# Performance work log

Measured on AMD Instinct MI355X. Metric: run time of the kernel, lower is better.

## Reference

```python
import jax, jax.numpy as jnp
import numpy as np

N = 50000       # nodes
E = 1600000     # edges (before self-loops)
H = 4           # heads
C = 32          # channels per head
G = 64          # graphs in batch
NEG_SLOPE = 0.2


def gat_conv(x, src, dst, W, att_src, att_dst, bias):
    # x: [N, Fin]; W: [Fin, H*C]; att_*: [H, C]; bias: [H*C]
    h = (x @ W).reshape(N, H, C)                       # [N, H, C]
    a_src = jnp.einsum('nhc,hc->nh', h, att_src)       # [N, H]
    a_dst = jnp.einsum('nhc,hc->nh', h, att_dst)       # [N, H]
    e = a_src[src] + a_dst[dst]                        # [E', H]
    e = jax.nn.leaky_relu(e, NEG_SLOPE)
    # softmax over incoming edges of each destination node
    m = jax.ops.segment_max(e, dst, num_segments=N)    # [N, H]
    ex = jnp.exp(e - m[dst])
    denom = jax.ops.segment_sum(ex, dst, num_segments=N)  # [N, H]
    alpha = ex / (denom[dst] + 1e-16)                  # [E', H]
    msg = h[src] * alpha[:, :, None]                   # [E', H, C]
    out = jax.ops.segment_sum(msg, dst, num_segments=N)  # [N, H, C]
    return out.reshape(N, H * C) + bias


def setup_inputs() -> dict:
    key = jax.random.key(0)
    ks = jax.random.split(key, 12)
    x = jax.random.normal(ks[0], (N, 128), dtype=jnp.float32)
    edge_index = jax.random.randint(ks[1], (2, E), 0, N, dtype=jnp.int64)
    batch = jnp.sort(jax.random.randint(ks[2], (N,), 0, G, dtype=jnp.int64))
    s = 0.05
    return {
        'x': x,
        'edge_index': edge_index,
        'batch': batch,
        'W1': jax.random.normal(ks[3], (128, H * C), dtype=jnp.float32) * s,
        'att_src1': jax.random.normal(ks[4], (H, C), dtype=jnp.float32) * s,
        'att_dst1': jax.random.normal(ks[5], (H, C), dtype=jnp.float32) * s,
        'b1': jnp.zeros((H * C,), dtype=jnp.float32),
        'W2': jax.random.normal(ks[6], (H * C, H * C), dtype=jnp.float32) * s,
        'att_src2': jax.random.normal(ks[7], (H, C), dtype=jnp.float32) * s,
        'att_dst2': jax.random.normal(ks[8], (H, C), dtype=jnp.float32) * s,
        'b2': jnp.zeros((H * C,), dtype=jnp.float32),
        'fc_W': jax.random.normal(ks[9], (H * C, 8), dtype=jnp.float32) * s,
        'fc_b': jnp.zeros((8,), dtype=jnp.float32),
    }


def reference(x, edge_index, batch, W1, att_src1, att_dst1, b1,
              W2, att_src2, att_dst2, b2, fc_W, fc_b):
    # add self loops (PyG GATConv default)
    ar = jnp.arange(N, dtype=edge_index.dtype)
    src = jnp.concatenate([edge_index[0], ar])
    dst = jnp.concatenate([edge_index[1], ar])
    h = gat_conv(x, src, dst, W1, att_src1, att_dst1, b1)
    h = jax.nn.elu(h)
    h = gat_conv(h, src, dst, W2, att_src2, att_dst2, b2)
    # global mean pool over graphs
    sums = jax.ops.segment_sum(h, batch, num_segments=G)          # [G, HC]
    cnt = jax.ops.segment_sum(jnp.ones((N,), h.dtype), batch, num_segments=G)
    pooled = sums / jnp.maximum(cnt, 1.0)[:, None]
    logits = pooled @ fc_W + fc_b                                  # [G, 8]
    return jax.nn.log_softmax(logits, axis=1)
```

## Files before the change

### kernel.cpp

```cpp
#include <hip/hip_runtime.h>
#include <math.h>

#define HC 128
#define GG 64
#define NEG 0.2f
#define TILE 8192
#define BW 128
#define SLOT 8192
#define NBMAX 512
#define LDA 136

typedef __attribute__((ext_vector_type(8))) short short8;
typedef __attribute__((ext_vector_type(4))) float floatx4;
typedef __attribute__((ext_vector_type(2))) float floatx2;

static __device__ __forceinline__ float leaky(float x) { return x > 0.f ? x : NEG * x; }

static __device__ __forceinline__ unsigned short f2bf(float f) {
    unsigned u = __float_as_uint(f);
    u += 0x7FFF + ((u >> 16) & 1);
    return (unsigned short)(u >> 16);
}
static __device__ __forceinline__ float bf2f(unsigned short s) {
    return __uint_as_float(((unsigned)s) << 16);
}

#if __has_builtin(__builtin_amdgcn_cvt_pk_f32_fp8) && __has_builtin(__builtin_amdgcn_cvt_pk_fp8_f32)
template <bool HI>
static __device__ __forceinline__ floatx2 fp8pair(unsigned int w) {
    return __builtin_amdgcn_cvt_pk_f32_fp8((int)w, HI);
}
static __device__ __forceinline__ unsigned int f32x2_fp8(float a, float b) {
    return ((unsigned int)__builtin_amdgcn_cvt_pk_fp8_f32(a, b, 0, false)) & 0xFFFFu;
}
#else
static __device__ __forceinline__ float fp8one(unsigned v) {
    unsigned e = (v >> 3) & 15u, m = v & 7u;
    float mag = e ? __uint_as_float(((e + 120u) << 23) | (m << 20))
                  : (float)m * 0.001953125f;
    return (v & 0x80u) ? -mag : mag;
}
template <bool HI>
static __device__ __forceinline__ floatx2 fp8pair(unsigned int w) {
    unsigned h = HI ? (w >> 16) : w;
    floatx2 r; r.x = fp8one(h & 0xFFu); r.y = fp8one((h >> 8) & 0xFFu);
    return r;
}
static __device__ __forceinline__ unsigned fp8enc(float f) {
    unsigned u = __float_as_uint(f);
    unsigned s = (u >> 24) & 0x80u;
    float a = fabsf(f);
    if (a >= 448.f) return s | 0x7Eu;
    if (a < 0.015625f) {
        unsigned m = (unsigned)(int)rintf(a * 512.f);
        return s | m;
    }
    u = __float_as_uint(a);
    u += 0xFFFFFu + ((u >> 20) & 1u);
    unsigned e8 = (u >> 23) - 120u;
    if (e8 >= 16u) return s | 0x7Eu;
    return s | (e8 << 3) | ((u >> 20) & 7u);
}
static __device__ __forceinline__ unsigned int f32x2_fp8(float a, float b) {
    return fp8enc(a) | (fp8enc(b) << 8);
}
#endif

static __device__ __forceinline__ void acc16(floatx2* acc, float w, const uint4& d) {
    floatx2 w2 = {w, w};
    acc[0] += w2 * fp8pair<false>(d.x);
    acc[1] += w2 * fp8pair<true>(d.x);
    acc[2] += w2 * fp8pair<false>(d.y);
    acc[3] += w2 * fp8pair<true>(d.y);
    acc[4] += w2 * fp8pair<false>(d.z);
    acc[5] += w2 * fp8pair<true>(d.z);
    acc[6] += w2 * fp8pair<false>(d.w);
    acc[7] += w2 * fp8pair<true>(d.w);
}

__global__ __launch_bounds__(256) void setup_k(const float* __restrict__ W1,
                                               const float* __restrict__ W2,
                                               unsigned short* __restrict__ Wt1,
                                               unsigned short* __restrict__ Wt2,
                                               int* __restrict__ gbcur,
                                               const int* __restrict__ batch,
                                               int* __restrict__ node_end,
                                               int* __restrict__ row_start,
                                               int NB, int Nn, int M) {
    int i = blockIdx.x * 256 + threadIdx.x;
    if (i < NB) gbcur[i] = i * SLOT;
    if (i == 0) row_start[Nn] = M;
    if (i < 32768) {
        const float* W = (i >> 14) ? W2 : W1;
        unsigned short* Wt = (i >> 14) ? Wt2 : Wt1;
        int d = i & 16383;
        int j = d & 7;
        int m = (d >> 3) & 15;
        int qf = d >> 7;
        int q = qf & 3;
        int f = qf >> 2;
        int kb = f & 3;
        int ct = f >> 2;
        int n = ct * 16 + m;
        int k = kb * 32 + q * 8 + j;
        Wt[d] = f2bf(W[k * 128 + n]);
    }
    if (i < Nn) {
        int b = batch[i];
        if (i == 0) {
            for (int g = 0; g < b; g++) node_end[g] = 0;
        }
        int bn = (i + 1 < Nn) ? batch[i + 1] : GG;
        for (int g = b; g < bn; g++) node_end[g] = i + 1;
    }
}

__global__ __launch_bounds__(256) void fused_k(const int* __restrict__ ei,
                                               int* __restrict__ gbcur,
                                               unsigned int* __restrict__ staging,
                                               int E, int M, int NB, int NBIN,
                                               const float* __restrict__ X,
                                               const unsigned short* __restrict__ Wt,
                                               const float* __restrict__ att_s,
                                               const float* __restrict__ att_d,
                                               unsigned char* __restrict__ H8,
                                               float* __restrict__ a_src,
                                               float* __restrict__ a_dst,
                                               int n_rows) {
    __shared__ __align__(16) char smem[39040];
    const int tid = threadIdx.x;

    if ((int)blockIdx.x < NBIN) {
        unsigned int* reorder = (unsigned int*)smem;
        int* s_cnt  = (int*)(smem + 32768);
        int* s_off  = (int*)(smem + 34816);
        int* s_run  = (int*)(smem + 36864);
        int* s_wsum = (int*)(smem + 38912);
        int* s_carry= (int*)(smem + 38944);
        const int lane = tid & 63, wid = tid >> 6;
        const int tbase = blockIdx.x * TILE;
        const int tcnt = min(TILE, M - tbase);

        for (int i = tid; i < NB; i += 256) s_cnt[i] = 0;
        if (tid == 0) *s_carry = 0;
        __syncthreads();

        for (int t = tid; t < tcnt; t += 256) {
            int i = tbase + t;
            int dst = (i < E) ? ei[E + i] : (i - E);
            atomicAdd(&s_cnt[dst >> 7], 1);
        }
        __syncthreads();

        for (int base = 0; base < NB; base += 256) {
            int i = base + tid;
            int v = (i < NB) ? s_cnt[i] : 0;
            int incl = v;
            #pragma unroll
            for (int off = 1; off < 64; off <<= 1) {
                int u = __shfl_up(incl, off);
                if (lane >= off) incl += u;
            }
            if (lane == 63) s_wsum[wid] = incl;
            __syncthreads();
            if (tid == 0) {
                int a = 0;
                for (int w = 0; w < 4; w++) { int tv = s_wsum[w]; s_wsum[w] = a; a += tv; }
                s_wsum[4] = a;
            }
            __syncthreads();
            int excl = *s_carry + s_wsum[wid] + incl - v;
            if (i < NB) s_off[i] = excl;
            __syncthreads();
            if (tid == 0) *s_carry += s_wsum[4];
            __syncthreads();
        }

        for (int b = tid; b < NB; b += 256)
            s_run[b] = atomicAdd(&gbcur[b], s_cnt[b]);
        for (int b = tid; b < NB; b += 256) s_cnt[b] = s_off[b];
        __syncthreads();

        for (int t = tid; t < tcnt; t += 256) {
            int i = tbase + t;
            int src, dst;
            if (i < E) { src = ei[i]; dst = ei[E + i]; }
            else       { src = dst = i - E; }
            unsigned int p = ((unsigned int)dst << 16) | (unsigned int)src;
            int r = atomicAdd(&s_cnt[dst >> 7], 1);
            reorder[r] = p;
        }
        __syncthreads();

        for (int t = tid; t < tcnt; t += 256) {
            unsigned int p = reorder[t];
            int b = p >> 23;
            staging[s_run[b] + (t - s_off[b])] = p;
        }
    } else {
        unsigned short* As = (unsigned short*)smem;
        const int gb = blockIdx.x - NBIN;
        const int row0 = gb * 64;

        for (int i = tid; i < 2048; i += 256) {
            int r = i >> 5;
            int c4 = (i & 31) << 2;
            int gr = row0 + r;
            float4 v = (gr < n_rows) ? ((const float4*)&X[(size_t)gr * 128])[i & 31]
                                     : make_float4(0.f, 0.f, 0.f, 0.f);
            ushort4 bv = {f2bf(v.x), f2bf(v.y), f2bf(v.z), f2bf(v.w)};
            *(ushort4*)&As[r * LDA + c4] = bv;
        }
        __syncthreads();

        const int lane = tid & 63;
        const int wave = tid >> 6;
        const int m = lane & 15;
        const int quad = lane >> 4;
        const int wr = wave * 16;

        floatx4 acc[8];
        #pragma unroll
        for (int ct = 0; ct < 8; ct++) acc[ct] = (floatx4){0.f, 0.f, 0.f, 0.f};

        #pragma unroll
        for (int kb = 0; kb < 4; kb++) {
            short8 x0 = *(const short8*)&As[(wr + m) * LDA + kb * 32 + quad * 8];
            #pragma unroll
            for (int ct = 0; ct < 8; ct++) {
                short8 wf = *(const short8*)&Wt[(((ct * 4 + kb) * 4) + quad) * 128 + m * 8];
                acc[ct] = __builtin_amdgcn_mfma_f32_16x16x32_bf16(wf, x0, acc[ct], 0, 0, 0);
            }
        }

        const int q4 = quad * 4;
        int node = row0 + wr + m;
        bool vld = node < n_rows;
        float ps[4] = {0.f, 0.f, 0.f, 0.f};
        float pd[4] = {0.f, 0.f, 0.f, 0.f};
        #pragma unroll
        for (int ct = 0; ct < 8; ct++) {
            floatx4 v = acc[ct];
            int c0 = ct * 16 + q4;
            float4 avs = *(const float4*)&att_s[c0];
            float4 avd = *(const float4*)&att_d[c0];
            int h = ct >> 1;
            ps[h] += v[0] * avs.x + v[1] * avs.y + v[2] * avs.z + v[3] * avs.w;
            pd[h] += v[0] * avd.x + v[1] * avd.y + v[2] * avd.z + v[3] * avd.w;
            if (vld) {
                unsigned pk01 = f32x2_fp8(v[0], v[1]);
                unsigned pk23 = f32x2_fp8(v[2], v[3]);
                *(unsigned*)&H8[(size_t)node * 128 + c0] = pk01 | (pk23 << 16);
            }
        }
        #pragma unroll
        for (int h = 0; h < 4; h++) {
            ps[h] += __shfl_xor(ps[h], 16); ps[h] += __shfl_xor(ps[h], 32);
            pd[h] += __shfl_xor(pd[h], 16); pd[h] += __shfl_xor(pd[h], 32);
        }
        if (lane < 16 && vld) {
            float4 s4 = {ps[0], ps[1], ps[2], ps[3]};
            float4 d4 = {pd[0], pd[1], pd[2], pd[3]};
            *(float4*)&a_src[node * 4] = s4;
            *(float4*)&a_dst[node * 4] = d4;
        }
    }
}

__global__ __launch_bounds__(256) void unbin_k(const unsigned int* __restrict__ staging,
                                               const int* __restrict__ gbcur,
                                               int* __restrict__ row_start,
                                               unsigned short* __restrict__ srcs, int Nn) {
    __shared__ int s_cnt[BW];
    __shared__ int s_cur[BW];
    __shared__ int s_w[4];
    int b = blockIdx.x, t = threadIdx.x;
    int sbase = b * SLOT;
    int cnt = gbcur[b] - sbase;

    int pacc = 0;
    for (int i = t; i < b; i += 256) pacc += gbcur[i] - i * SLOT;
    #pragma unroll
    for (int off = 1; off < 64; off <<= 1) pacc += __shfl_xor(pacc, off);
    if ((t & 63) == 0) s_w[t >> 6] = pacc;
    __syncthreads();
    int bb = s_w[0] + s_w[1] + s_w[2] + s_w[3];
    __syncthreads();

    int n0 = b * BW;
    if (t < BW) s_cnt[t] = 0;
    __syncthreads();
    for (int j = t; j < cnt; j += 256)
        atomicAdd(&s_cnt[(staging[sbase + j] >> 16) & (BW - 1)], 1);
    __syncthreads();
    int v = (t < BW) ? s_cnt[t] : 0;
    int incl = v;
    #pragma unroll
    for (int off = 1; off < 64; off <<= 1) {
        int u = __shfl_up(incl, off);
        if ((t & 63) >= off) incl += u;
    }
    if (t < BW && (t & 63) == 63) s_w[t >> 6] = incl;
    __syncthreads();
    int excl = incl - v + ((t >= 64 && t < BW) ? s_w[0] : 0);
    if (t < BW) {
        s_cur[t] = bb + excl;
        if (n0 + t < Nn) row_start[n0 + t] = bb + excl;
    }
    __syncthreads();
    for (int j = t; j < cnt; j += 256) {
        unsigned int p = staging[sbase + j];
        int ln = (int)(p >> 16) & (BW - 1);
        int r = atomicAdd(&s_cur[ln], 1);
        srcs[r] = (unsigned short)(p & 0xFFFFu);
    }
}

__global__ __launch_bounds__(128) void gemm_fused(const unsigned short* __restrict__ X,
                                                  const unsigned short* __restrict__ Wt,
                                                  const float* __restrict__ att_s,
                                                  const float* __restrict__ att_d,
                                                  unsigned char* __restrict__ H8,
                                                  float* __restrict__ a_src,
                                                  float* __restrict__ a_dst,
                                                  int n_rows) {
    __shared__ unsigned short As[64 * LDA];
    const int tid = threadIdx.x;
    const int row0 = blockIdx.x * 64;

    for (int i = tid; i < 1024; i += 128) {
        int r = i >> 4;
        int c8 = (i & 15) << 3;
        int gr = row0 + r;
        uint4 v = (gr < n_rows) ? *(const uint4*)&X[(size_t)gr * 128 + c8]
                                : make_uint4(0, 0, 0, 0);
        *(uint4*)&As[r * LDA + c8] = v;
    }
    __syncthreads();

    const int lane = tid & 63;
    const int wave = tid >> 6;
    const int m = lane & 15;
    const int quad = lane >> 4;
    const int wr0 = wave * 32;

    floatx4 acc[2][8];
    #pragma unroll
    for (int nt = 0; nt < 2; nt++)
        #pragma unroll
        for (int ct = 0; ct < 8; ct++)
            acc[nt][ct] = (floatx4){0.f, 0.f, 0.f, 0.f};

    #pragma unroll
    for (int kb = 0; kb < 4; kb++) {
        short8 x0 = *(const short8*)&As[(wr0 + m) * LDA + kb * 32 + quad * 8];
        short8 x1 = *(const short8*)&As[(wr0 + 16 + m) * LDA + kb * 32 + quad * 8];
        #pragma unroll
        for (int ct = 0; ct < 8; ct++) {
            short8 wf = *(const short8*)&Wt[(((ct * 4 + kb) * 4) + quad) * 128 + m * 8];
            acc[0][ct] = __builtin_amdgcn_mfma_f32_16x16x32_bf16(wf, x0, acc[0][ct], 0, 0, 0);
            acc[1][ct] = __builtin_amdgcn_mfma_f32_16x16x32_bf16(wf, x1, acc[1][ct], 0, 0, 0);
        }
    }

    const int q4 = quad * 4;
    #pragma unroll
    for (int nt = 0; nt < 2; nt++) {
        int node = row0 + wr0 + nt * 16 + m;
        bool vld = node < n_rows;
        float ps[4] = {0.f, 0.f, 0.f, 0.f};
        float pd[4] = {0.f, 0.f, 0.f, 0.f};
        #pragma unroll
        for (int ct = 0; ct < 8; ct++) {
            floatx4 v = acc[nt][ct];
            int c0 = ct * 16 + q4;
            float4 avs = *(const float4*)&att_s[c0];
            float4 avd = *(const float4*)&att_d[c0];
            int h = ct >> 1;
            ps[h] += v[0] * avs.x + v[1] * avs.y + v[2] * avs.z + v[3] * avs.w;
            pd[h] += v[0] * avd.x + v[1] * avd.y + v[2] * avd.z + v[3] * avd.w;
            if (vld) {
                unsigned pk01 = f32x2_fp8(v[0], v[1]);
                unsigned pk23 = f32x2_fp8(v[2], v[3]);
                *(unsigned*)&H8[(size_t)node * 128 + c0] = pk01 | (pk23 << 16);
            }
        }
        #pragma unroll
        for (int h = 0; h < 4; h++) {
            ps[h] += __shfl_xor(ps[h], 16); ps[h] += __shfl_xor(ps[h], 32);
            pd[h] += __shfl_xor(pd[h], 16); pd[h] += __shfl_xor(pd[h], 32);
        }
        if (lane < 16 && vld) {
            float4 s4 = {ps[0], ps[1], ps[2], ps[3]};
            float4 d4 = {pd[0], pd[1], pd[2], pd[3]};
            *(float4*)&a_src[node * 4] = s4;
            *(float4*)&a_dst[node * 4] = d4;
        }
    }
}

__global__ __launch_bounds__(256) void gat_agg(const unsigned char* __restrict__ H8,
                                               const float* __restrict__ a_src,
                                               const float* __restrict__ a_dst,
                                               const int* __restrict__ row_start,
                                               const unsigned short* __restrict__ srcs,
                                               const float* __restrict__ bias,
                                               unsigned short* __restrict__ OUT,
                                               const int* __restrict__ batch,
                                               float* __restrict__ partial,
                                               int n_rows, int mode) {
    __shared__ float ls[32][128];
    __shared__ int sg[32];
    int n = (blockIdx.x * 256 + threadIdx.x) >> 3;
    int li = threadIdx.x & 7;
    int hd = li >> 1;
    bool vld = n < n_rows;

    float o[16];
    #pragma unroll
    for (int k = 0; k < 16; k++) o[k] = 0.f;

    if (vld) {
        int base = row_start[n];
        int end = row_start[n + 1];
        float adh = a_dst[n * 4 + hd];

        floatx2 acc[8];
        #pragma unroll
        for (int k = 0; k < 8; k++) acc[k] = (floatx2){0.f, 0.f};
        float wsum = 0.f;

        int j = base;
        int head_n = min(end - j, (4 - (base & 3)) & 3);
        for (int q = 0; q < head_n; q++, j++) {
            int s0 = srcs[j];
            float w0 = __expf(leaky(a_src[s0 * 4 + hd] + adh));
            uint4 d0 = *(const uint4*)&H8[(size_t)s0 * 128 + li * 16];
            acc16(acc, w0, d0);
            wsum += w0;
        }
        for (; j + 4 <= end; j += 4) {
            uint2 sv = *(const uint2*)&srcs[j];
            int s0 = sv.x & 0xFFFFu, s1 = sv.x >> 16;
            int s2 = sv.y & 0xFFFFu, s3 = sv.y >> 16;
            float a0 = a_src[s0 * 4 + hd];
            float a1 = a_src[s1 * 4 + hd];
            float a2 = a_src[s2 * 4 + hd];
            float a3 = a_src[s3 * 4 + hd];
            uint4 d0 = *(const uint4*)&H8[(size_t)s0 * 128 + li * 16];
            uint4 d1 = *(const uint4*)&H8[(size_t)s1 * 128 + li * 16];
            uint4 d2 = *(const uint4*)&H8[(size_t)s2 * 128 + li * 16];
            uint4 d3 = *(const uint4*)&H8[(size_t)s3 * 128 + li * 16];
            float w0 = __expf(leaky(a0 + adh));
            float w1 = __expf(leaky(a1 + adh));
            float w2 = __expf(leaky(a2 + adh));
            float w3 = __expf(leaky(a3 + adh));
            acc16(acc, w0, d0);
            acc16(acc, w1, d1);
            acc16(acc, w2, d2);
            acc16(acc, w3, d3);
            wsum += (w0 + w1) + (w2 + w3);
        }
        for (; j < end; j++) {
            int s0 = srcs[j];
            float w0 = __expf(leaky(a_src[s0 * 4 + hd] + adh));
            uint4 d0 = *(const uint4*)&H8[(size_t)s0 * 128 + li * 16];
            acc16(acc, w0, d0);
            wsum += w0;
        }

        float ih = 1.0f / (wsum + 1e-16f);
        #pragma unroll
        for (int k = 0; k < 8; k++) {
            float2 bv = *(const float2*)&bias[li * 16 + 2 * k];
            o[2 * k]     = acc[k].x * ih + bv.x;
            o[2 * k + 1] = acc[k].y * ih + bv.y;
        }
    }

    if (mode == 0) {
        if (vld) {
            #pragma unroll
            for (int k = 0; k < 16; k++) o[k] = o[k] > 0.f ? o[k] : __expf(o[k]) - 1.f;
            unsigned int pk[8];
            #pragma unroll
            for (int k = 0; k < 8; k++)
                pk[k] = ((unsigned)f2bf(o[2 * k + 1]) << 16) | (unsigned)f2bf(o[2 * k]);
            uint4 s0v = {pk[0], pk[1], pk[2], pk[3]};
            uint4 s1v = {pk[4], pk[5], pk[6], pk[7]};
            unsigned short* op = &OUT[(size_t)n * 128 + li * 16];
            *(uint4*)op = s0v;
            *(uint4*)(op + 8) = s1v;
        }
    } else {
        int nl = threadIdx.x >> 3;
        int n0b = blockIdx.x * 32;
        float* row = &ls[nl][li * 16];
        *(float4*)&row[0]  = (float4){o[0], o[1], o[2], o[3]};
        *(float4*)&row[4]  = (float4){o[4], o[5], o[6], o[7]};
        *(float4*)&row[8]  = (float4){o[8], o[9], o[10], o[11]};
        *(float4*)&row[12] = (float4){o[12], o[13], o[14], o[15]};
        if (li == 0) sg[nl] = vld ? min(batch[n] - batch[n0b], 3) : 0;
        __syncthreads();
        int t = threadIdx.x;
        if (t < 128) {
            float a0 = 0.f, a1 = 0.f, a2 = 0.f, a3 = 0.f;
            #pragma unroll 8
            for (int r = 0; r < 32; r++) {
                float v = ls[r][t];
                int gr = sg[r];
                a0 += (gr == 0) ? v : 0.f;
                a1 += (gr == 1) ? v : 0.f;
                a2 += (gr == 2) ? v : 0.f;
                a3 += (gr == 3) ? v : 0.f;
            }
            float* pp = &partial[(size_t)blockIdx.x * 4 * 128];
            pp[t] = a0;
            pp[128 + t] = a1;
            pp[256 + t] = a2;
            pp[384 + t] = a3;
        }
    }
}

__global__ __launch_bounds__(64) void head_k(const float* __restrict__ partial,
                                             const int* __restrict__ node_end,
                                             const int* __restrict__ batch,
                                             const float* __restrict__ fcW,
                                             const float* __restrict__ fcb,
                                             float* __restrict__ out, int n_rows) {
    __shared__ float p[128];
    __shared__ float lg[8];
    int g = blockIdx.x, t = threadIdx.x;
    int s = (g > 0) ? node_end[g - 1] : 0;
    int e = node_end[g];
    float cnt = fmaxf((float)(e - s), 1.0f);
    float v0 = 0.f, v1 = 0.f;
    if (e > s) {
        int b0 = s >> 5;
        int b1 = (e - 1) >> 5;
        for (int b = b0; b <= b1; b++) {
            int slot = g - batch[b * 32];
            if (slot < 0 || slot > 3) continue;
            const float* pp = &partial[((size_t)b * 4 + slot) * 128];
            v0 += pp[t];
            v1 += pp[64 + t];
        }
    }
    p[t] = v0 / cnt;
    p[t + 64] = v1 / cnt;
    __syncthreads();
    if (t < 8) {
        float sacc = fcb[t];
        for (int k = 0; k < 128; k++) sacc += p[k] * fcW[k * 8 + t];
        lg[t] = sacc;
    }
    __syncthreads();
    if (t == 0) {
        float m = lg[0];
        for (int j = 1; j < 8; j++) m = fmaxf(m, lg[j]);
        float se = 0.f;
        for (int j = 0; j < 8; j++) se += expf(lg[j] - m);
        float lse = logf(se) + m;
        for (int j = 0; j < 8; j++) out[g * 8 + j] = lg[j] - lse;
    }
}

extern "C" void kernel_launch(void* const* d_in, const int* in_sizes, int n_in,
                              void* d_out, int out_size, void* d_ws, size_t ws_size,
                              hipStream_t stream) {
    const float* x    = (const float*)d_in[0];
    const int*   ei   = (const int*)d_in[1];
    const int*   batch= (const int*)d_in[2];
    const float* W1   = (const float*)d_in[3];
    const float* as1  = (const float*)d_in[4];
    const float* ad1  = (const float*)d_in[5];
    const float* b1   = (const float*)d_in[6];
    const float* W2   = (const float*)d_in[7];
    const float* as2  = (const float*)d_in[8];
    const float* ad2  = (const float*)d_in[9];
    const float* b2   = (const float*)d_in[10];
    const float* fcW  = (const float*)d_in[11];
    const float* fcb  = (const float*)d_in[12];
    float* out = (float*)d_out;

    const int Nn = in_sizes[0] / HC;
    const int E  = in_sizes[1] / 2;
    const int M  = E + Nn;
    const int NB = (Nn + BW - 1) / BW;
    const int NBIN = (M + TILE - 1) / TILE;
    const int GB1 = (Nn + 63) / 64;
    const int NBLK2 = (Nn + 31) / 32;

    char* ws = (char*)d_ws;
    size_t off = 0;
    auto alloc = [&](size_t bytes) -> char* {
        char* p = ws + off;
        off = (off + bytes + 255) & ~(size_t)255;
        return p;
    };
    size_t hB_bytes  = (size_t)Nn * HC * 2;
    size_t stg_bytes = (size_t)NB * SLOT * 4;
    char* hB_region = alloc(hB_bytes > stg_bytes ? hB_bytes : stg_bytes);
    unsigned short* hB      = (unsigned short*)hB_region;
    unsigned int*   staging = (unsigned int*)hB_region;
    unsigned char*  H8      = (unsigned char*)alloc((size_t)Nn * HC);
    float* asrc      = (float*)alloc((size_t)Nn * 4 * 4);
    float* adst      = (float*)alloc((size_t)Nn * 4 * 4);
    unsigned short* srcs = (unsigned short*)alloc((size_t)M * 2);
    int*   row_start = (int*)alloc((size_t)(Nn + 1) * 4);
    float* partial   = (float*)alloc((size_t)NBLK2 * 4 * HC * 4);
    int*   node_end  = (int*)alloc((size_t)GG * 4);
    int*   gbcur     = (int*)alloc((size_t)NB * 4);
    unsigned short* Wt1 = (unsigned short*)alloc(16384 * 2);
    unsigned short* Wt2 = (unsigned short*)alloc(16384 * 2);

    setup_k<<<(Nn + 255) / 256, 256, 0, stream>>>(W1, W2, Wt1, Wt2, gbcur, batch,
                                                  node_end, row_start, NB, Nn, M);
    fused_k<<<NBIN + GB1, 256, 0, stream>>>(ei, gbcur, staging, E, M, NB, NBIN,
                                            x, Wt1, as1, ad1, H8, asrc, adst, Nn);
    unbin_k<<<NB, 256, 0, stream>>>(staging, gbcur, row_start, srcs, Nn);
    gat_agg<<<NBLK2, 256, 0, stream>>>(H8, asrc, adst, row_start, srcs, b1, hB,
                                       batch, partial, Nn, 0);
    gemm_fused<<<GB1, 128, 0, stream>>>(hB, Wt2, as2, ad2, H8, asrc, adst, Nn);
    gat_agg<<<NBLK2, 256, 0, stream>>>(H8, asrc, adst, row_start, srcs, b2, hB,
                                       batch, partial, Nn, 1);
    head_k<<<GG, 64, 0, stream>>>(partial, node_end, batch, fcW, fcb, out, Nn);
}
```

Measured before the change: 245.1 us.

## Replace two-pass binned CSR build with degree-count, scan and atomic scatter

Replaces the tiled bucket-binning sort (shared-memory binning into staging slots, then per-bucket unbinning) with a direct CSR build. It counts per-node in-degree with global atomics, runs a three-kernel exclusive scan, then scatters source ids using per-node atomic cursors. The aim is to drop the staging buffer traffic and the heavy shared-memory scans. In exchange it adds about 1.65M contended global atomics twice, two extra small kernel launches, and a nondeterministic edge order within each row.

New measurement: 416.6 us. 1.7x slower.

```diff
diff --git a/kernel.cpp b/kernel.cpp
--- a/kernel.cpp
+++ b/kernel.cpp
@@ -4,11 +4,8 @@
 #define HC 128
 #define GG 64
 #define NEG 0.2f
-#define TILE 8192
-#define BW 128
-#define SLOT 8192
-#define NBMAX 512
 #define LDA 136
+#define NH 256
 
 typedef __attribute__((ext_vector_type(8))) short short8;
 typedef __attribute__((ext_vector_type(4))) float floatx4;
@@ -20,9 +17,6 @@
     unsigned u = __float_as_uint(f);
     u += 0x7FFF + ((u >> 16) & 1);
     return (unsigned short)(u >> 16);
-}
-static __device__ __forceinline__ float bf2f(unsigned short s) {
-    return __uint_as_float(((unsigned)s) << 16);
 }
 
 #if __has_builtin(__builtin_amdgcn_cvt_pk_f32_fp8) && __has_builtin(__builtin_amdgcn_cvt_pk_fp8_f32)
@@ -82,13 +76,12 @@
                                                const float* __restrict__ W2,
                                                unsigned short* __restrict__ Wt1,
                                                unsigned short* __restrict__ Wt2,
-                                               int* __restrict__ gbcur,
+                                               int* __restrict__ deg,
                                                const int* __restrict__ batch,
                                                int* __restrict__ node_end,
                                                int* __restrict__ row_start,
-                                               int NB, int Nn, int M) {
+                                               int Nn, int M) {
     int i = blockIdx.x * 256 + threadIdx.x;
-    if (i < NB) gbcur[i] = i * SLOT;
     if (i == 0) row_start[Nn] = M;
     if (i < 32768) {
         const float* W = (i >> 14) ? W2 : W1;
@@ -106,6 +99,7 @@
         Wt[d] = f2bf(W[k * 128 + n]);
     }
     if (i < Nn) {
+        deg[i] = 0;
         int b = batch[i];
         if (i == 0) {
             for (int g = 0; g < b; g++) node_end[g] = 0;
@@ -116,9 +110,8 @@
 }
 
 __global__ __launch_bounds__(256) void fused_k(const int* __restrict__ ei,
-                                               int* __restrict__ gbcur,
-                                               unsigned int* __restrict__ staging,
-                                               int E, int M, int NB, int NBIN,
+                                               int* __restrict__ deg,
+                                               int E, int M,
                                                const float* __restrict__ X,
                                                const unsigned short* __restrict__ Wt,
                                                const float* __restrict__ att_s,
@@ -127,79 +120,17 @@
                                                float* __restrict__ a_src,
                                                float* __restrict__ a_dst,
                                                int n_rows) {
-    __shared__ __align__(16) char smem[39040];
+    __shared__ __align__(16) unsigned short As[64 * LDA];
     const int tid = threadIdx.x;
 
-    if ((int)blockIdx.x < NBIN) {
-        unsigned int* reorder = (unsigned int*)smem;
-        int* s_cnt  = (int*)(smem + 32768);
-        int* s_off  = (int*)(smem + 34816);
-        int* s_run  = (int*)(smem + 36864);
-        int* s_wsum = (int*)(smem + 38912);
-        int* s_carry= (int*)(smem + 38944);
-        const int lane = tid & 63, wid = tid >> 6;
-        const int tbase = blockIdx.x * TILE;
-        const int tcnt = min(TILE, M - tbase);
-
-        for (int i = tid; i < NB; i += 256) s_cnt[i] = 0;
-        if (tid == 0) *s_carry = 0;
-        __syncthreads();
-
-        for (int t = tid; t < tcnt; t += 256) {
-            int i = tbase + t;
+    if ((int)blockIdx.x < NH) {
+        const int stride = NH * 256;
+        for (int i = blockIdx.x * 256 + tid; i < M; i += stride) {
             int dst = (i < E) ? ei[E + i] : (i - E);
-            atomicAdd(&s_cnt[dst >> 7], 1);
-        }
-        __syncthreads();
-
-        for (int base = 0; base < NB; base += 256) {
-            int i = base + tid;
-            int v = (i < NB) ? s_cnt[i] : 0;
-            int incl = v;
-            #pragma unroll
-            for (int off = 1; off < 64; off <<= 1) {
-                int u = __shfl_up(incl, off);
-                if (lane >= off) incl += u;
-            }
-            if (lane == 63) s_wsum[wid] = incl;
-            __syncthreads();
-            if (tid == 0) {
-                int a = 0;
-                for (int w = 0; w < 4; w++) { int tv = s_wsum[w]; s_wsum[w] = a; a += tv; }
-                s_wsum[4] = a;
-            }
-            __syncthreads();
-            int excl = *s_carry + s_wsum[wid] + incl - v;
-            if (i < NB) s_off[i] = excl;
-            __syncthreads();
-            if (tid == 0) *s_carry += s_wsum[4];
-            __syncthreads();
-        }
-
-        for (int b = tid; b < NB; b += 256)
-            s_run[b] = atomicAdd(&gbcur[b], s_cnt[b]);
-        for (int b = tid; b < NB; b += 256) s_cnt[b] = s_off[b];
-        __syncthreads();
-
-        for (int t = tid; t < tcnt; t += 256) {
-            int i = tbase + t;
-            int src, dst;
-            if (i < E) { src = ei[i]; dst = ei[E + i]; }
-            else       { src = dst = i - E; }
-            unsigned int p = ((unsigned int)dst << 16) | (unsigned int)src;
-            int r = atomicAdd(&s_cnt[dst >> 7], 1);
-            reorder[r] = p;
-        }
-        __syncthreads();
-
-        for (int t = tid; t < tcnt; t += 256) {
-            unsigned int p = reorder[t];
-            int b = p >> 23;
-            staging[s_run[b] + (t - s_off[b])] = p;
+            atomicAdd(&deg[dst], 1);
         }
     } else {
-        unsigned short* As = (unsigned short*)smem;
-        const int gb = blockIdx.x - NBIN;
+        const int gb = blockIdx.x - NH;
         const int row0 = gb * 64;
 
         for (int i = tid; i < 2048; i += 256) {
@@ -267,52 +198,78 @@
     }
 }
 
-__global__ __launch_bounds__(256) void unbin_k(const unsigned int* __restrict__ staging,
-                                               const int* __restrict__ gbcur,
-                                               int* __restrict__ row_start,
-                                               unsigned short* __restrict__ srcs, int Nn) {
-    __shared__ int s_cnt[BW];
-    __shared__ int s_cur[BW];
-    __shared__ int s_w[4];
-    int b = blockIdx.x, t = threadIdx.x;
-    int sbase = b * SLOT;
-    int cnt = gbcur[b] - sbase;
-
-    int pacc = 0;
-    for (int i = t; i < b; i += 256) pacc += gbcur[i] - i * SLOT;
+__global__ __launch_bounds__(512) void scan_sums_k(const int* __restrict__ deg,
+                                                   int* __restrict__ sums, int Nn) {
+    __shared__ int w[8];
+    int t = threadIdx.x;
+    int i = blockIdx.x * 512 + t;
+    int v = (i < Nn) ? deg[i] : 0;
     #pragma unroll
-    for (int off = 1; off < 64; off <<= 1) pacc += __shfl_xor(pacc, off);
-    if ((t & 63) == 0) s_w[t >> 6] = pacc;
-    __syncthreads();
-    int bb = s_w[0] + s_w[1] + s_w[2] + s_w[3];
-    __syncthreads();
-
-    int n0 = b * BW;
-    if (t < BW) s_cnt[t] = 0;
-    __syncthreads();
-    for (int j = t; j < cnt; j += 256)
-        atomicAdd(&s_cnt[(staging[sbase + j] >> 16) & (BW - 1)], 1);
-    __syncthreads();
-    int v = (t < BW) ? s_cnt[t] : 0;
+    for (int off = 1; off < 64; off <<= 1) v += __shfl_xor(v, off);
+    if ((t & 63) == 0) w[t >> 6] = v;
+    __syncthreads();
+    if (t == 0) {
+        int s = 0;
+        #pragma unroll
+        for (int k = 0; k < 8; k++) s += w[k];
+        sums[blockIdx.x] = s;
+    }
+}
+
+__global__ __launch_bounds__(128) void scan_base_k(int* __restrict__ sums, int NS) {
+    __shared__ int buf[128];
+    int t = threadIdx.x;
+    if (t < NS) buf[t] = sums[t];
+    __syncthreads();
+    if (t == 0) {
+        int run = 0;
+        for (int k = 0; k < NS; k++) { int v = buf[k]; buf[k] = run; run += v; }
+    }
+    __syncthreads();
+    if (t < NS) sums[t] = buf[t];
+}
+
+__global__ __launch_bounds__(512) void scan_write_k(const int* __restrict__ deg,
+                                                    const int* __restrict__ bases,
+                                                    int* __restrict__ row_start,
+                                                    int* __restrict__ cur, int Nn) {
+    __shared__ int ws[8];
+    int t = threadIdx.x;
+    int lane = t & 63, wid = t >> 6;
+    int i = blockIdx.x * 512 + t;
+    int v = (i < Nn) ? deg[i] : 0;
     int incl = v;
     #pragma unroll
     for (int off = 1; off < 64; off <<= 1) {
         int u = __shfl_up(incl, off);
-        if ((t & 63) >= off) incl += u;
-    }
-    if (t < BW && (t & 63) == 63) s_w[t >> 6] = incl;
-    __syncthreads();
-    int excl = incl - v + ((t >= 64 && t < BW) ? s_w[0] : 0);
-    if (t < BW) {
-        s_cur[t] = bb + excl;
-        if (n0 + t < Nn) row_start[n0 + t] = bb + excl;
-    }
-    __syncthreads();
-    for (int j = t; j < cnt; j += 256) {
-        unsigned int p = staging[sbase + j];
-        int ln = (int)(p >> 16) & (BW - 1);
-        int r = atomicAdd(&s_cur[ln], 1);
-        srcs[r] = (unsigned short)(p & 0xFFFFu);
+        if (lane >= off) incl += u;
+    }
+    if (lane == 63) ws[wid] = incl;
+    __syncthreads();
+    if (t == 0) {
+        int run = 0;
+        #pragma unroll
+        for (int k = 0; k < 8; k++) { int s = ws[k]; ws[k] = run; run += s; }
+    }
+    __syncthreads();
+    int rs = bases[blockIdx.x] + ws[wid] + incl - v;
+    if (i < Nn) {
+        row_start[i] = rs;
+        cur[i] = rs;
+    }
+}
+
+__global__ __launch_bounds__(256) void scatter_k(const int* __restrict__ ei,
+                                                 int* __restrict__ cur,
+                                                 unsigned short* __restrict__ srcs,
+                                                 int E, int M) {
+    int stride = gridDim.x * 256;
+    for (int i = blockIdx.x * 256 + threadIdx.x; i < M; i += stride) {
+        int src, dst;
+        if (i < E) { src = ei[i]; dst = ei[E + i]; }
+        else       { src = dst = i - E; }
+        int r = atomicAdd(&cur[dst], 1);
+        srcs[r] = (unsigned short)src;
     }
 }
 
@@ -587,10 +544,9 @@
     const int Nn = in_sizes[0] / HC;
     const int E  = in_sizes[1] / 2;
     const int M  = E + Nn;
-    const int NB = (Nn + BW - 1) / BW;
-    const int NBIN = (M + TILE - 1) / TILE;
     const int GB1 = (Nn + 63) / 64;
     const int NBLK2 = (Nn + 31) / 32;
+    const int NS = (Nn + 511) / 512;
 
     char* ws = (char*)d_ws;
     size_t off = 0;
@@ -599,27 +555,28 @@
         off = (off + bytes + 255) & ~(size_t)255;
         return p;
     };
-    size_t hB_bytes  = (size_t)Nn * HC * 2;
-    size_t stg_bytes = (size_t)NB * SLOT * 4;
-    char* hB_region = alloc(hB_bytes > stg_bytes ? hB_bytes : stg_bytes);
-    unsigned short* hB      = (unsigned short*)hB_region;
-    unsigned int*   staging = (unsigned int*)hB_region;
-    unsigned char*  H8      = (unsigned char*)alloc((size_t)Nn * HC);
+    unsigned short* hB = (unsigned short*)alloc((size_t)Nn * HC * 2);
+    unsigned char*  H8 = (unsigned char*)alloc((size_t)Nn * HC);
     float* asrc      = (float*)alloc((size_t)Nn * 4 * 4);
     float* adst      = (float*)alloc((size_t)Nn * 4 * 4);
     unsigned short* srcs = (unsigned short*)alloc((size_t)M * 2);
     int*   row_start = (int*)alloc((size_t)(Nn + 1) * 4);
+    int*   deg       = (int*)alloc((size_t)Nn * 4);
+    int*   cur       = (int*)alloc((size_t)Nn * 4);
+    int*   sums      = (int*)alloc((size_t)128 * 4);
     float* partial   = (float*)alloc((size_t)NBLK2 * 4 * HC * 4);
     int*   node_end  = (int*)alloc((size_t)GG * 4);
-    int*   gbcur     = (int*)alloc((size_t)NB * 4);
     unsigned short* Wt1 = (unsigned short*)alloc(16384 * 2);
     unsigned short* Wt2 = (unsigned short*)alloc(16384 * 2);
 
-    setup_k<<<(Nn + 255) / 256, 256, 0, stream>>>(W1, W2, Wt1, Wt2, gbcur, batch,
-                                                  node_end, row_start, NB, Nn, M);
-    fused_k<<<NBIN + GB1, 256, 0, stream>>>(ei, gbcur, staging, E, M, NB, NBIN,
-                                            x, Wt1, as1, ad1, H8, asrc, adst, Nn);
-    unbin_k<<<NB, 256, 0, stream>>>(staging, gbcur, row_start, srcs, Nn);
+    setup_k<<<(Nn + 255) / 256, 256, 0, stream>>>(W1, W2, Wt1, Wt2, deg, batch,
+                                                  node_end, row_start, Nn, M);
+    fused_k<<<NH + GB1, 256, 0, stream>>>(ei, deg, E, M,
+                                          x, Wt1, as1, ad1, H8, asrc, adst, Nn);
+    scan_sums_k<<<NS, 512, 0, stream>>>(deg, sums, Nn);
+    scan_base_k<<<1, 128, 0, stream>>>(sums, NS);
+    scan_write_k<<<NS, 512, 0, stream>>>(deg, sums, row_start, cur, Nn);
+    scatter_k<<<512, 256, 0, stream>>>(ei, cur, srcs, E, M);
     gat_agg<<<NBLK2, 256, 0, stream>>>(H8, asrc, adst, row_start, srcs, b1, hB,
                                        batch, partial, Nn, 0);
     gemm_fused<<<GB1, 128, 0, stream>>>(hB, Wt2, as2, ad2, H8, asrc, adst, Nn);
```
